# Kernel optimization log

Hardware: AMD Instinct MI355X
Metric: run time of the kernel (lower is better)

Reference implementation:

```python
import jax, jax.numpy as jnp
import numpy as np

D_MODEL = 1024
NUM_HEADS = 16
HEAD_DIM = D_MODEL // NUM_HEADS  # 64


def setup_inputs() -> dict:
    key = jax.random.key(0)
    ks = jax.random.split(key, 9)
    s = 1.0 / np.sqrt(D_MODEL)
    return {
        "x": jax.random.normal(ks[0], (2, 2048, D_MODEL), dtype=jnp.float32),
        "Wq": jax.random.normal(ks[1], (D_MODEL, D_MODEL), dtype=jnp.float32) * s,
        "bq": jnp.zeros((D_MODEL,), dtype=jnp.float32),
        "Wk": jax.random.normal(ks[2], (D_MODEL, HEAD_DIM), dtype=jnp.float32) * s,
        "bk": jnp.zeros((HEAD_DIM,), dtype=jnp.float32),
        "Wv": jax.random.normal(ks[3], (D_MODEL, HEAD_DIM), dtype=jnp.float32) * s,
        "bv": jnp.zeros((HEAD_DIM,), dtype=jnp.float32),
        "Wo": jax.random.normal(ks[4], (D_MODEL, D_MODEL), dtype=jnp.float32) * s,
        "bo": jnp.zeros((D_MODEL,), dtype=jnp.float32),
    }


def reference(x, Wq, bq, Wk, bk, Wv, bv, Wo, bo):
    B, S, D = x.shape
    H, hd = NUM_HEADS, HEAD_DIM
    # Projections: Q has H heads, K/V a single shared head (MQA).
    Q = (x @ Wq + bq).reshape(B, S, H, hd).transpose(0, 2, 1, 3)  # [B,H,S,hd]
    K = x @ Wk + bk  # [B,S,hd]
    V = x @ Wv + bv  # [B,S,hd]
    # Shared-K/V attention: broadcast K across heads instead of expand().
    scores = jnp.einsum("bhqd,bkd->bhqk", Q, K) / np.sqrt(hd)  # [B,H,S,S]
    attn = jax.nn.softmax(scores, axis=-1)
    attended = jnp.einsum("bhqk,bkd->bhqd", attn, V)  # [B,H,S,hd]
    attended = attended.transpose(0, 2, 1, 3).reshape(B, S, D)
    return attended @ Wo + bo
```

## Files before the change

### kernel.cpp

```cpp
#include <hip/hip_runtime.h>
#include <hip/hip_bf16.h>

#define D_MODEL 1024
#define NHEADS  16
#define HD      64
#define BATCH   2
#define SEQ     2048
#define MROWS   4096
#define NQKV    1152

typedef short  short4v __attribute__((ext_vector_type(4)));
typedef short  short8  __attribute__((ext_vector_type(8)));
typedef float  floatx4 __attribute__((ext_vector_type(4)));
typedef unsigned uint4v __attribute__((ext_vector_type(4)));

__device__ inline short f2bf(float f) {
  unsigned u = __builtin_bit_cast(unsigned, f);
  u = (u + 0x7FFF + ((u >> 16) & 1)) >> 16;
  return (short)u;
}

__device__ inline unsigned pack_trunc(float lo, float hi) {
  return __builtin_amdgcn_perm(__builtin_bit_cast(unsigned, hi),
                               __builtin_bit_cast(unsigned, lo), 0x07060302u);
}

__device__ inline void async_copy16(const short* g, short* l) {
  __builtin_amdgcn_global_load_lds(
      (const __attribute__((address_space(1))) unsigned int*)g,
      (__attribute__((address_space(3))) unsigned int*)l, 16, 0, 0);
}

__global__ __launch_bounds__(256)
void prep_kernel(const float* __restrict__ x,  const float* __restrict__ Wq,
                 const float* __restrict__ Wk, const float* __restrict__ Wv,
                 const float* __restrict__ Wo, const float* __restrict__ bq,
                 const float* __restrict__ bk, const float* __restrict__ bv,
                 short* __restrict__ xb, short* __restrict__ Wqkv_t,
                 short* __restrict__ Wo_t, float* __restrict__ bqkv) {
  const int id = blockIdx.x;
  const int t  = threadIdx.x;
  if (id < 544) {
    __shared__ short Ts[64 * 72];
    const float* src; short* dst; int N, off, tile;
    if (id < 256)      { src = Wq; dst = Wqkv_t; N = 1024; off = 0;    tile = id; }
    else if (id < 272) { src = Wk; dst = Wqkv_t; N = 64;   off = 1024; tile = id - 256; }
    else if (id < 288) { src = Wv; dst = Wqkv_t; N = 64;   off = 1088; tile = id - 272; }
    else               { src = Wo; dst = Wo_t;   N = 1024; off = 0;    tile = id - 288; }
    const int k0 = (N == 1024) ? (tile & 15) * 64 : tile * 64;
    const int n0 = (N == 1024) ? (tile >> 4) * 64 : 0;
    {
      const int r = t >> 2, c = (t & 3) * 16;
      const float* s = src + (size_t)(k0 + r) * N + n0 + c;
#pragma unroll
      for (int j = 0; j < 16; j += 4) {
        float4 v = *reinterpret_cast<const float4*>(s + j);
        Ts[r * 72 + c + j + 0] = f2bf(v.x); Ts[r * 72 + c + j + 1] = f2bf(v.y);
        Ts[r * 72 + c + j + 2] = f2bf(v.z); Ts[r * 72 + c + j + 3] = f2bf(v.w);
      }
    }
    __syncthreads();
    {
      const int n = t >> 2, kc = (t & 3) * 16;
      short8 o0, o1;
#pragma unroll
      for (int j = 0; j < 8; ++j) o0[j] = Ts[(kc + j) * 72 + n];
#pragma unroll
      for (int j = 0; j < 8; ++j) o1[j] = Ts[(kc + 8 + j) * 72 + n];
      short* d = dst + (size_t)(off + n0 + n) * 1024 + k0 + kc;
      *reinterpret_cast<short8*>(d)     = o0;
      *reinterpret_cast<short8*>(d + 8) = o1;
    }
  } else if (id < 549) {
    const int i = (id - 544) * 256 + t;
    if (i < 1024)      bqkv[i] = bq[i];
    else if (i < 1088) bqkv[i] = bk[i - 1024];
    else if (i < 1152) bqkv[i] = bv[i - 1088];
  } else {
    const int i = ((id - 549) * 256 + t) * 8;
    if (i < MROWS * D_MODEL) {
      float4 a = *reinterpret_cast<const float4*>(x + i);
      float4 b = *reinterpret_cast<const float4*>(x + i + 4);
      short8 o;
      o[0] = f2bf(a.x); o[1] = f2bf(a.y); o[2] = f2bf(a.z); o[3] = f2bf(a.w);
      o[4] = f2bf(b.x); o[5] = f2bf(b.y); o[6] = f2bf(b.z); o[7] = f2bf(b.w);
      *reinterpret_cast<short8*>(xb + i) = o;
    }
  }
}

template<bool OUT_BF16, int SCALE_N, bool VT_FUSE>
__global__ __launch_bounds__(256)
void gemm_mfma_bt(const short* __restrict__ A, const short* __restrict__ Bt,
                  const float* __restrict__ bias, void* __restrict__ Cout,
                  short* __restrict__ Vtg, int M, int N, int K) {
  __shared__ short As[2][128 * 64];
  __shared__ short Bs[2][64 * 64];
  const int t    = threadIdx.x;
  const int w    = t >> 6;
  const int lane = t & 63;
  const int quad = lane >> 4;
  const int l16  = lane & 15;
  const int bm   = blockIdx.x * 128;
  const int bn   = blockIdx.y * 64;
  const int wm   = (w >> 1) * 64;
  const int wn   = (w & 1) * 32;

  const int srow = t >> 3;
  const int cc   = ((t & 7) ^ (srow & 7)) * 8;
  const short* gA = A  + (size_t)(bm + srow) * K + cc;
  const short* gB = Bt + (size_t)(bn + srow) * K + cc;

  floatx4 acc[4][2];
#pragma unroll
  for (int i = 0; i < 4; ++i)
#pragma unroll
    for (int j = 0; j < 2; ++j) acc[i][j] = (floatx4){0.f, 0.f, 0.f, 0.f};

  const int xr = l16 & 7;

  async_copy16(gA, &As[0][t * 8]);
  async_copy16(gA + (size_t)32 * K, &As[0][t * 8 + 2048]);
  async_copy16(gA + (size_t)64 * K, &As[0][t * 8 + 4096]);
  async_copy16(gA + (size_t)96 * K, &As[0][t * 8 + 6144]);
  async_copy16(gB, &Bs[0][t * 8]);
  async_copy16(gB + (size_t)32 * K, &Bs[0][t * 8 + 2048]);

  int cur = 0;
  for (int k0 = 0; k0 < K; k0 += 64) {
    asm volatile("s_waitcnt vmcnt(0)" ::: "memory");
    __builtin_amdgcn_s_barrier();
    __builtin_amdgcn_sched_barrier(0);

    if (k0 + 64 < K) {
      const int nb = cur ^ 1;
      const int kn = k0 + 64;
      async_copy16(gA + kn, &As[nb][t * 8]);
      async_copy16(gA + (size_t)32 * K + kn, &As[nb][t * 8 + 2048]);
      async_copy16(gA + (size_t)64 * K + kn, &As[nb][t * 8 + 4096]);
      async_copy16(gA + (size_t)96 * K + kn, &As[nb][t * 8 + 6144]);
      async_copy16(gB + kn, &Bs[nb][t * 8]);
      async_copy16(gB + (size_t)32 * K + kn, &Bs[nb][t * 8 + 2048]);
    }
    __builtin_amdgcn_sched_barrier(0);

    const short* Ac = As[cur];
    const short* Bc = Bs[cur];
    short8 fa0[4], fa1[4], fb0[2], fb1[2];
#pragma unroll
    for (int mi = 0; mi < 4; ++mi) {
      const int row = wm + mi * 16 + l16;
      fa0[mi] = *reinterpret_cast<const short8*>(&Ac[row * 64 + (quad ^ xr) * 8]);
      fa1[mi] = *reinterpret_cast<const short8*>(&Ac[row * 64 + ((4 + quad) ^ xr) * 8]);
    }
#pragma unroll
    for (int ni = 0; ni < 2; ++ni) {
      const int row = wn + ni * 16 + l16;
      fb0[ni] = *reinterpret_cast<const short8*>(&Bc[row * 64 + (quad ^ xr) * 8]);
      fb1[ni] = *reinterpret_cast<const short8*>(&Bc[row * 64 + ((4 + quad) ^ xr) * 8]);
    }
#pragma unroll
    for (int mi = 0; mi < 4; ++mi)
#pragma unroll
      for (int ni = 0; ni < 2; ++ni) {
        acc[mi][ni] = __builtin_amdgcn_mfma_f32_16x16x32_bf16(fa0[mi], fb0[ni], acc[mi][ni], 0, 0, 0);
        acc[mi][ni] = __builtin_amdgcn_mfma_f32_16x16x32_bf16(fa1[mi], fb1[ni], acc[mi][ni], 0, 0, 0);
      }
    cur ^= 1;
  }

#pragma unroll
  for (int ni = 0; ni < 2; ++ni) {
    const int col = bn + wn + ni * 16 + l16;
    const float bs = bias[col];
    const float sc = (col < SCALE_N) ? 0.18033688f : 1.0f;
#pragma unroll
    for (int mi = 0; mi < 4; ++mi) {
      const int row = bm + wm + mi * 16 + quad * 4;
      short4v vt4;
#pragma unroll
      for (int r = 0; r < 4; ++r) {
        const float v = (acc[mi][ni][r] + bs) * sc;
        if (OUT_BF16) {
          const short bv16 = f2bf(v);
          ((short*)Cout)[(size_t)(row + r) * N + col] = bv16;
          if (VT_FUSE) vt4[r] = bv16;
        } else {
          ((float*)Cout)[(size_t)(row + r) * N + col] = v;
        }
      }
      if (VT_FUSE && col >= 1088) {
        const int d = col - 1088;
        const int b = row >> 11, s = row & 2047;
        *reinterpret_cast<short4v*>(&Vtg[(size_t)(b * 64 + d) * SEQ + s]) = vt4;
      }
    }
  }
}

__global__ __launch_bounds__(256, 2)
void mqa_flash_bf16(const short* __restrict__ QKV, const short* __restrict__ Vtg,
                    short* __restrict__ Att) {
  const int bh   = blockIdx.y;
  const int b    = bh >> 4;
  const int h    = bh & 15;
  const int s0   = blockIdx.x * 128;
  const int t    = threadIdx.x;
  const int w    = t >> 6;
  const int lane = t & 63;
  const int quad = lane >> 4;
  const int l16  = lane & 15;

  __shared__ short KVs[2][16384];

  short8 aq[2][2];
#pragma unroll
  for (int st = 0; st < 2; ++st) {
    const short* qrow = &QKV[(size_t)(b * SEQ + s0 + w * 32 + st * 16 + l16) * NQKV + h * HD];
    aq[st][0] = *reinterpret_cast<const short8*>(qrow + quad * 8);
    aq[st][1] = *reinterpret_cast<const short8*>(qrow + 32 + quad * 8);
  }

  floatx4 oacc[2][4];
  floatx4 lacc[2];
#pragma unroll
  for (int st = 0; st < 2; ++st) {
    lacc[st] = (floatx4){0.f, 0.f, 0.f, 0.f};
#pragma unroll
    for (int dg = 0; dg < 4; ++dg) oacc[st][dg] = (floatx4){0.f, 0.f, 0.f, 0.f};
  }

  short8 ones;
#pragma unroll
  for (int j = 0; j < 8; ++j) ones[j] = (short)0x3F80;

  const int srow = t >> 3;
  const int cc   = ((t & 7) ^ (srow & 7)) * 8;
  const int krow = ((srow >> 4) & 1) * 4 + ((srow >> 2) & 3) * 8 + (srow & 3);
  const short* gK = QKV + (size_t)(b * SEQ + krow) * NQKV + 1024 + cc;
  const short* gV = Vtg + (size_t)(b * 64 + srow) * SEQ + cc;

  const int xr = l16 & 7;

#define STAGE(BUF)                                                     \
  {                                                                    \
    short* lK  = KVs[BUF] + w * 512;                                   \
    short* lV0 = KVs[BUF] + 8192  + w * 512;                           \
    short* lV1 = KVs[BUF] + 12288 + w * 512;                           \
    async_copy16(gK, lK);                                              \
    async_copy16(gK + (size_t)32 * NQKV, lK + 2048);                   \
    async_copy16(gK + (size_t)64 * NQKV, lK + 4096);                   \
    async_copy16(gK + (size_t)96 * NQKV, lK + 6144);                   \
    async_copy16(gV, lV0);                                             \
    async_copy16(gV + (size_t)32 * SEQ, lV0 + 2048);                   \
    async_copy16(gV + 64, lV1);                                        \
    async_copy16(gV + (size_t)32 * SEQ + 64, lV1 + 2048);              \
    gK += (size_t)128 * NQKV;                                          \
    gV += 128;                                                         \
  }

  STAGE(0)

  const int NT = SEQ / 128;
  int cur = 0;

  for (int it = 0; it < NT; ++it) {
    asm volatile("s_waitcnt vmcnt(0)" ::: "memory");
    __builtin_amdgcn_s_barrier();
    __builtin_amdgcn_sched_barrier(0);

    if (it + 1 < NT) STAGE(cur ^ 1)
    __builtin_amdgcn_sched_barrier(0);

#pragma unroll
    for (int half = 0; half < 2; ++half) {
      const short* Ks = KVs[cur] + half * 4096;
      const short* Vt = KVs[cur] + 8192 + half * 4096;

      short8 kb[4][2], vb[4][2];
#pragma unroll
      for (int kg = 0; kg < 4; ++kg) {
        kb[kg][0] = *reinterpret_cast<const short8*>(&Ks[(kg * 16 + l16) * 64 + (quad ^ xr) * 8]);
        kb[kg][1] = *reinterpret_cast<const short8*>(&Ks[(kg * 16 + l16) * 64 + ((4 + quad) ^ xr) * 8]);
      }
#pragma unroll
      for (int dg = 0; dg < 4; ++dg) {
        vb[dg][0] = *reinterpret_cast<const short8*>(&Vt[(dg * 16 + l16) * 64 + (quad ^ xr) * 8]);
        vb[dg][1] = *reinterpret_cast<const short8*>(&Vt[(dg * 16 + l16) * 64 + ((4 + quad) ^ xr) * 8]);
      }

#pragma unroll
      for (int st = 0; st < 2; ++st) {
        floatx4 s4[4];
#pragma unroll
        for (int kg = 0; kg < 4; ++kg) {
          s4[kg] = (floatx4){0.f, 0.f, 0.f, 0.f};
          s4[kg] = __builtin_amdgcn_mfma_f32_16x16x32_bf16(kb[kg][0], aq[st][0], s4[kg], 0, 0, 0);
          s4[kg] = __builtin_amdgcn_mfma_f32_16x16x32_bf16(kb[kg][1], aq[st][1], s4[kg], 0, 0, 0);
        }
        unsigned pk[8];
#pragma unroll
        for (int kg = 0; kg < 4; ++kg) {
          const float p0 = __builtin_exp2f(s4[kg][0]);
          const float p1 = __builtin_exp2f(s4[kg][1]);
          const float p2 = __builtin_exp2f(s4[kg][2]);
          const float p3 = __builtin_exp2f(s4[kg][3]);
          pk[kg * 2 + 0] = pack_trunc(p0, p1);
          pk[kg * 2 + 1] = pack_trunc(p2, p3);
        }
        const uint4v u0 = (uint4v){pk[0], pk[1], pk[2], pk[3]};
        const uint4v u1 = (uint4v){pk[4], pk[5], pk[6], pk[7]};
        const short8 ap0 = __builtin_bit_cast(short8, u0);
        const short8 ap1 = __builtin_bit_cast(short8, u1);

        __builtin_amdgcn_s_setprio(1);
        lacc[st] = __builtin_amdgcn_mfma_f32_16x16x32_bf16(ap0, ones, lacc[st], 0, 0, 0);
        lacc[st] = __builtin_amdgcn_mfma_f32_16x16x32_bf16(ap1, ones, lacc[st], 0, 0, 0);
#pragma unroll
        for (int dg = 0; dg < 4; ++dg) {
          oacc[st][dg] = __builtin_amdgcn_mfma_f32_16x16x32_bf16(ap0, vb[dg][0], oacc[st][dg], 0, 0, 0);
          oacc[st][dg] = __builtin_amdgcn_mfma_f32_16x16x32_bf16(ap1, vb[dg][1], oacc[st][dg], 0, 0, 0);
        }
        __builtin_amdgcn_s_setprio(0);
      }
    }
    cur ^= 1;
  }
#undef STAGE

  short* At = Att + (size_t)b * SEQ * D_MODEL + h * HD;
#pragma unroll
  for (int st = 0; st < 2; ++st) {
#pragma unroll
    for (int rg = 0; rg < 4; ++rg) {
      const int q = s0 + w * 32 + st * 16 + quad * 4 + rg;
      const float inv = 1.0f / lacc[st][rg];
      short* dst = At + (size_t)q * D_MODEL + l16;
#pragma unroll
      for (int dg = 0; dg < 4; ++dg) dst[dg * 16] = f2bf(oacc[st][dg][rg] * inv);
    }
  }
}

extern "C" void kernel_launch(void* const* d_in, const int* in_sizes, int n_in,
                              void* d_out, int out_size, void* d_ws, size_t ws_size,
                              hipStream_t stream) {
  const float* x  = (const float*)d_in[0];
  const float* Wq = (const float*)d_in[1];
  const float* bq = (const float*)d_in[2];
  const float* Wk = (const float*)d_in[3];
  const float* bk = (const float*)d_in[4];
  const float* Wv = (const float*)d_in[5];
  const float* bv = (const float*)d_in[6];
  const float* Wo = (const float*)d_in[7];
  const float* bo = (const float*)d_in[8];
  float* out = (float*)d_out;

  short* Wqkv_t = (short*)d_ws;
  short* Wo_t   = Wqkv_t + (size_t)NQKV * D_MODEL;
  short* xb     = Wo_t + (size_t)D_MODEL * D_MODEL;
  short* QKV    = xb + (size_t)MROWS * D_MODEL;
  short* Att    = QKV + (size_t)MROWS * NQKV;
  short* Vtg    = Att + (size_t)MROWS * D_MODEL;
  float* bqkv   = (float*)(Vtg + (size_t)BATCH * HD * SEQ);

  prep_kernel<<<2597, 256, 0, stream>>>(x, Wq, Wk, Wv, Wo, bq, bk, bv,
                                        xb, Wqkv_t, Wo_t, bqkv);

  gemm_mfma_bt<true, 1024, true><<<dim3(MROWS / 128, NQKV / 64), 256, 0, stream>>>(
      xb, Wqkv_t, bqkv, QKV, Vtg, MROWS, NQKV, D_MODEL);

  mqa_flash_bf16<<<dim3(SEQ / 128, BATCH * NHEADS), 256, 0, stream>>>(
      QKV, Vtg, Att);

  gemm_mfma_bt<false, 0, false><<<dim3(MROWS / 128, D_MODEL / 64), 256, 0, stream>>>(
      Att, Wo_t, bo, out, nullptr, MROWS, D_MODEL, D_MODEL);
}
```

Before: 166.1 us.

## Load K/V fragments directly from global memory instead of staging through LDS

```diff
diff --git a/kernel.cpp b/kernel.cpp
--- a/kernel.cpp
+++ b/kernel.cpp
@@ -211,8 +211,6 @@
   const int quad = lane >> 4;
   const int l16  = lane & 15;
 
-  __shared__ short KVs[2][16384];
-
   short8 aq[2][2];
 #pragma unroll
   for (int st = 0; st < 2; ++st) {
@@ -234,99 +232,71 @@
 #pragma unroll
   for (int j = 0; j < 8; ++j) ones[j] = (short)0x3F80;
 
-  const int srow = t >> 3;
-  const int cc   = ((t & 7) ^ (srow & 7)) * 8;
-  const int krow = ((srow >> 4) & 1) * 4 + ((srow >> 2) & 3) * 8 + (srow & 3);
-  const short* gK = QKV + (size_t)(b * SEQ + krow) * NQKV + 1024 + cc;
-  const short* gV = Vtg + (size_t)(b * 64 + srow) * SEQ + cc;
-
-  const int xr = l16 & 7;
-
-#define STAGE(BUF)                                                     \
-  {                                                                    \
-    short* lK  = KVs[BUF] + w * 512;                                   \
-    short* lV0 = KVs[BUF] + 8192  + w * 512;                           \
-    short* lV1 = KVs[BUF] + 12288 + w * 512;                           \
-    async_copy16(gK, lK);                                              \
-    async_copy16(gK + (size_t)32 * NQKV, lK + 2048);                   \
-    async_copy16(gK + (size_t)64 * NQKV, lK + 4096);                   \
-    async_copy16(gK + (size_t)96 * NQKV, lK + 6144);                   \
-    async_copy16(gV, lV0);                                             \
-    async_copy16(gV + (size_t)32 * SEQ, lV0 + 2048);                   \
-    async_copy16(gV + 64, lV1);                                        \
-    async_copy16(gV + (size_t)32 * SEQ + 64, lV1 + 2048);              \
-    gK += (size_t)128 * NQKV;                                          \
-    gV += 128;                                                         \
-  }
-
-  STAGE(0)
-
-  const int NT = SEQ / 128;
-  int cur = 0;
-
-  for (int it = 0; it < NT; ++it) {
-    asm volatile("s_waitcnt vmcnt(0)" ::: "memory");
-    __builtin_amdgcn_s_barrier();
-    __builtin_amdgcn_sched_barrier(0);
-
-    if (it + 1 < NT) STAGE(cur ^ 1)
-    __builtin_amdgcn_sched_barrier(0);
-
-#pragma unroll
-    for (int half = 0; half < 2; ++half) {
-      const short* Ks = KVs[cur] + half * 4096;
-      const short* Vt = KVs[cur] + 8192 + half * 4096;
-
-      short8 kb[4][2], vb[4][2];
+  const int krl = ((l16 >> 2) & 3) * 8 + (l16 & 3);
+  const short* pK0 = QKV + (size_t)(b * SEQ + krl) * NQKV + 1024 + quad * 8;
+  const short* pK1 = pK0 + (size_t)4  * NQKV;
+  const short* pK2 = pK0 + (size_t)32 * NQKV;
+  const short* pK3 = pK0 + (size_t)36 * NQKV;
+  const short* pV0 = Vtg + (size_t)(b * 64 + l16) * SEQ + quad * 8;
+  const short* pV1 = pV0 + (size_t)16 * SEQ;
+  const short* pV2 = pV0 + (size_t)32 * SEQ;
+  const short* pV3 = pV0 + (size_t)48 * SEQ;
+
+  for (int kk = 0; kk < SEQ; kk += 64) {
+    const size_t ko = (size_t)kk * NQKV;
+    short8 kb[4][2], vb[4][2];
+    kb[0][0] = *reinterpret_cast<const short8*>(pK0 + ko);
+    kb[0][1] = *reinterpret_cast<const short8*>(pK0 + ko + 32);
+    kb[1][0] = *reinterpret_cast<const short8*>(pK1 + ko);
+    kb[1][1] = *reinterpret_cast<const short8*>(pK1 + ko + 32);
+    kb[2][0] = *reinterpret_cast<const short8*>(pK2 + ko);
+    kb[2][1] = *reinterpret_cast<const short8*>(pK2 + ko + 32);
+    kb[3][0] = *reinterpret_cast<const short8*>(pK3 + ko);
+    kb[3][1] = *reinterpret_cast<const short8*>(pK3 + ko + 32);
+    vb[0][0] = *reinterpret_cast<const short8*>(pV0 + kk);
+    vb[0][1] = *reinterpret_cast<const short8*>(pV0 + kk + 32);
+    vb[1][0] = *reinterpret_cast<const short8*>(pV1 + kk);
+    vb[1][1] = *reinterpret_cast<const short8*>(pV1 + kk + 32);
+    vb[2][0] = *reinterpret_cast<const short8*>(pV2 + kk);
+    vb[2][1] = *reinterpret_cast<const short8*>(pV2 + kk + 32);
+    vb[3][0] = *reinterpret_cast<const short8*>(pV3 + kk);
+    vb[3][1] = *reinterpret_cast<const short8*>(pV3 + kk + 32);
+
+#pragma unroll
+    for (int st = 0; st < 2; ++st) {
+      floatx4 s4[4];
 #pragma unroll
       for (int kg = 0; kg < 4; ++kg) {
-        kb[kg][0] = *reinterpret_cast<const short8*>(&Ks[(kg * 16 + l16) * 64 + (quad ^ xr) * 8]);
-        kb[kg][1] = *reinterpret_cast<const short8*>(&Ks[(kg * 16 + l16) * 64 + ((4 + quad) ^ xr) * 8]);
-      }
+        s4[kg] = (floatx4){0.f, 0.f, 0.f, 0.f};
+        s4[kg] = __builtin_amdgcn_mfma_f32_16x16x32_bf16(kb[kg][0], aq[st][0], s4[kg], 0, 0, 0);
+        s4[kg] = __builtin_amdgcn_mfma_f32_16x16x32_bf16(kb[kg][1], aq[st][1], s4[kg], 0, 0, 0);
+      }
+      unsigned pk[8];
+#pragma unroll
+      for (int kg = 0; kg < 4; ++kg) {
+        const float p0 = __builtin_exp2f(s4[kg][0]);
+        const float p1 = __builtin_exp2f(s4[kg][1]);
+        const float p2 = __builtin_exp2f(s4[kg][2]);
+        const float p3 = __builtin_exp2f(s4[kg][3]);
+        pk[kg * 2 + 0] = pack_trunc(p0, p1);
+        pk[kg * 2 + 1] = pack_trunc(p2, p3);
+      }
+      const uint4v u0 = (uint4v){pk[0], pk[1], pk[2], pk[3]};
+      const uint4v u1 = (uint4v){pk[4], pk[5], pk[6], pk[7]};
+      const short8 ap0 = __builtin_bit_cast(short8, u0);
+      const short8 ap1 = __builtin_bit_cast(short8, u1);
+
+      __builtin_amdgcn_s_setprio(1);
+      lacc[st] = __builtin_amdgcn_mfma_f32_16x16x32_bf16(ap0, ones, lacc[st], 0, 0, 0);
+      lacc[st] = __builtin_amdgcn_mfma_f32_16x16x32_bf16(ap1, ones, lacc[st], 0, 0, 0);
 #pragma unroll
       for (int dg = 0; dg < 4; ++dg) {
-        vb[dg][0] = *reinterpret_cast<const short8*>(&Vt[(dg * 16 + l16) * 64 + (quad ^ xr) * 8]);
-        vb[dg][1] = *reinterpret_cast<const short8*>(&Vt[(dg * 16 + l16) * 64 + ((4 + quad) ^ xr) * 8]);
-      }
-
-#pragma unroll
-      for (int st = 0; st < 2; ++st) {
-        floatx4 s4[4];
-#pragma unroll
-        for (int kg = 0; kg < 4; ++kg) {
-          s4[kg] = (floatx4){0.f, 0.f, 0.f, 0.f};
-          s4[kg] = __builtin_amdgcn_mfma_f32_16x16x32_bf16(kb[kg][0], aq[st][0], s4[kg], 0, 0, 0);
-          s4[kg] = __builtin_amdgcn_mfma_f32_16x16x32_bf16(kb[kg][1], aq[st][1], s4[kg], 0, 0, 0);
-        }
-        unsigned pk[8];
-#pragma unroll
-        for (int kg = 0; kg < 4; ++kg) {
-          const float p0 = __builtin_exp2f(s4[kg][0]);
-          const float p1 = __builtin_exp2f(s4[kg][1]);
-          const float p2 = __builtin_exp2f(s4[kg][2]);
-          const float p3 = __builtin_exp2f(s4[kg][3]);
-          pk[kg * 2 + 0] = pack_trunc(p0, p1);
-          pk[kg * 2 + 1] = pack_trunc(p2, p3);
-        }
-        const uint4v u0 = (uint4v){pk[0], pk[1], pk[2], pk[3]};
-        const uint4v u1 = (uint4v){pk[4], pk[5], pk[6], pk[7]};
-        const short8 ap0 = __builtin_bit_cast(short8, u0);
-        const short8 ap1 = __builtin_bit_cast(short8, u1);
-
-        __builtin_amdgcn_s_setprio(1);
-        lacc[st] = __builtin_amdgcn_mfma_f32_16x16x32_bf16(ap0, ones, lacc[st], 0, 0, 0);
-        lacc[st] = __builtin_amdgcn_mfma_f32_16x16x32_bf16(ap1, ones, lacc[st], 0, 0, 0);
-#pragma unroll
-        for (int dg = 0; dg < 4; ++dg) {
-          oacc[st][dg] = __builtin_amdgcn_mfma_f32_16x16x32_bf16(ap0, vb[dg][0], oacc[st][dg], 0, 0, 0);
-          oacc[st][dg] = __builtin_amdgcn_mfma_f32_16x16x32_bf16(ap1, vb[dg][1], oacc[st][dg], 0, 0, 0);
-        }
-        __builtin_amdgcn_s_setprio(0);
-      }
-    }
-    cur ^= 1;
-  }
-#undef STAGE
+        oacc[st][dg] = __builtin_amdgcn_mfma_f32_16x16x32_bf16(ap0, vb[dg][0], oacc[st][dg], 0, 0, 0);
+        oacc[st][dg] = __builtin_amdgcn_mfma_f32_16x16x32_bf16(ap1, vb[dg][1], oacc[st][dg], 0, 0, 0);
+      }
+      __builtin_amdgcn_s_setprio(0);
+    }
+  }
 
   short* At = Att + (size_t)b * SEQ * D_MODEL + h * HD;
 #pragma unroll
```

Measured after the change: 234.7 us. 1.41x slower.
